# Kernel optimization log

Hardware: AMD Instinct MI355X
Metric: run time of the kernel (lower is better)

## Reference

```python
import jax, jax.numpy as jnp
import numpy as np

B, T, D = 4, 2048, 1024
H = 16
HD = D // H  # 64

def setup_inputs() -> dict:
    key = jax.random.key(0)
    k1, k2, k3 = jax.random.split(key, 3)
    x = jax.random.normal(k1, (B, T, D), dtype=jnp.float32)
    # torch nn.Linear weight layout: [out_features, in_features]
    w_qkv = jax.random.normal(k2, (3 * D, D), dtype=jnp.float32) * (D ** -0.5)
    w_proj = jax.random.normal(k3, (D, D), dtype=jnp.float32) * (D ** -0.5)
    return {"x": x, "w_qkv": w_qkv, "w_proj": w_proj}

def reference(x, w_qkv, w_proj):
    b, t, c = x.shape
    qkv = jnp.einsum('btc,oc->bto', x, w_qkv)  # [b,t,3c]
    q, k, v = jnp.split(qkv, 3, axis=-1)
    # [b,h,t,hd]
    q = q.reshape(b, t, H, HD).transpose(0, 2, 1, 3)
    k = k.reshape(b, t, H, HD).transpose(0, 2, 1, 3)
    v = v.reshape(b, t, H, HD).transpose(0, 2, 1, 3)
    att = jnp.einsum('bhqd,bhkd->bhqk', q, k) / (HD ** 0.5)
    causal = jnp.tril(jnp.ones((t, t), dtype=bool))
    att = jnp.where(causal, att, -jnp.inf)
    att = jax.nn.softmax(att, axis=-1)
    y = jnp.einsum('bhqk,bhkd->bhqd', att, v)
    y = y.transpose(0, 2, 1, 3).reshape(b, t, c)
    return jnp.einsum('btc,oc->bto', y, w_proj)
```

## Files before the change

kernel.cpp:

```cpp
#include <hip/hip_runtime.h>
#include <cstdint>
#include <cstddef>


typedef __bf16 bf16;
typedef __bf16 bf16x8 __attribute__((ext_vector_type(8)));
typedef float  f32x4  __attribute__((ext_vector_type(4)));
typedef float  fvec4  __attribute__((ext_vector_type(4)));
typedef unsigned u32x4 __attribute__((ext_vector_type(4)));

typedef __attribute__((address_space(1))) const void global_cv;
typedef __attribute__((address_space(3))) void lds_v;

#define MFMA16(a, b, c) __builtin_amdgcn_mfma_f32_16x16x32_bf16((a), (b), (c), 0, 0, 0)

#define QSCALE 0.18033688f

__device__ __forceinline__ void async_ld16(const bf16* g, bf16* l) {
  __builtin_amdgcn_global_load_lds((global_cv*)g, (lds_v*)l, 16, 0, 0);
}

__device__ __forceinline__ int swz_off(int row, int col) {
  int sr = (row & 7) ^ ((row >> 3) & 7);
  return row * 64 + ((((col >> 3) ^ sr) & 7) * 8) + (col & 7);
}

__device__ __forceinline__ bf16x8 cvt8(const float* p) {
  fvec4 u = *(const fvec4*)p;
  fvec4 v = *(const fvec4*)(p + 4);
  bf16x8 r;
  r[0] = (bf16)u[0]; r[1] = (bf16)u[1]; r[2] = (bf16)u[2]; r[3] = (bf16)u[3];
  r[4] = (bf16)v[0]; r[5] = (bf16)v[1]; r[6] = (bf16)v[2]; r[7] = (bf16)v[3];
  return r;
}

__global__ void cvt_f32_bf16(const float* __restrict__ s, bf16* __restrict__ d,
                             int n8) {
  int i = blockIdx.x * 256 + threadIdx.x;
  if (i < n8) *(bf16x8*)(d + (size_t)i * 8) = cvt8(s + (size_t)i * 8);
}

__device__ __forceinline__ void qkv_scatter(const f32x4 acc[4][4], int m0, int n0,
                                            int wm, int wn, int quad, int l15,
                                            bf16* Qo, bf16* Ko, bf16* Vo) {
  const int which = n0 >> 10;
  bf16* dst = (which == 0) ? Qo : (which == 1) ? Ko : Vo;
  const float scale = (which == 0) ? QSCALE : 1.0f;
#pragma unroll
  for (int i = 0; i < 4; ++i) {
    const int m = m0 + wm + i * 16 + quad * 4;
#pragma unroll
    for (int j = 0; j < 4; ++j) {
      const int n  = n0 + wn + j * 16 + l15;
      const int n1 = n & 1023;
      const int h  = n1 >> 6;
      const int d  = n1 & 63;
#pragma unroll
      for (int r = 0; r < 4; ++r) {
        const int mm = m + r;
        const int b  = mm >> 11;
        const int t  = mm & 2047;
        dst[(((size_t)(b * 16 + h)) * 2048 + t) * 64 + d] =
            (bf16)(acc[i][j][r] * scale);
      }
    }
  }
}

__global__ __launch_bounds__(256, 2)
void gemm_qkv_a(const bf16* __restrict__ A, const bf16* __restrict__ B,
                bf16* __restrict__ Qo, bf16* __restrict__ Ko,
                bf16* __restrict__ Vo) {
  __shared__ __align__(16) bf16 As[128 * 32];
  __shared__ __align__(16) bf16 Bs[128 * 32];
  const int K = 1024;

  const int tid  = threadIdx.x;
  const int lane = tid & 63;
  const int wave = tid >> 6;
  const int quad = lane >> 4;
  const int l15  = lane & 15;
  const int wm   = (wave >> 1) * 64;
  const int wn   = (wave & 1) * 64;
  const int m0   = blockIdx.y * 128;
  const int n0   = blockIdx.x * 128;

  f32x4 acc[4][4];
#pragma unroll
  for (int i = 0; i < 4; ++i)
#pragma unroll
    for (int j = 0; j < 4; ++j) acc[i][j] = f32x4{0.f, 0.f, 0.f, 0.f};

  const int r0 = tid >> 2;
  const int c0 = (tid & 3) * 8;
  const bf16* ag0 = A + (size_t)(m0 + r0) * K + c0;
  const bf16* ag1 = A + (size_t)(m0 + 64 + r0) * K + c0;
  const bf16* bg0 = B + (size_t)(n0 + r0) * K + c0;
  const bf16* bg1 = B + (size_t)(n0 + 64 + r0) * K + c0;
  const int lo0 = (wave * 64) * 8;
  const int lo1 = (256 + wave * 64) * 8;

  for (int k0 = 0; k0 < K; k0 += 32) {
    __syncthreads();
    async_ld16(ag0 + k0, As + lo0);
    async_ld16(ag1 + k0, As + lo1);
    async_ld16(bg0 + k0, Bs + lo0);
    async_ld16(bg1 + k0, Bs + lo1);
    __syncthreads();

    bf16x8 af[4], bfr[4];
#pragma unroll
    for (int i = 0; i < 4; ++i)
      af[i] = *(const bf16x8*)(As + (wm + i * 16 + l15) * 32 + quad * 8);
#pragma unroll
    for (int j = 0; j < 4; ++j)
      bfr[j] = *(const bf16x8*)(Bs + (wn + j * 16 + l15) * 32 + quad * 8);
#pragma unroll
    for (int i = 0; i < 4; ++i)
#pragma unroll
      for (int j = 0; j < 4; ++j)
        acc[i][j] = MFMA16(af[i], bfr[j], acc[i][j]);
  }
  qkv_scatter(acc, m0, n0, wm, wn, quad, l15, Qo, Ko, Vo);
}

__global__ __launch_bounds__(256, 2)
void gemm_qkv_f(const float* __restrict__ A, const float* __restrict__ B,
                bf16* __restrict__ Qo, bf16* __restrict__ Ko,
                bf16* __restrict__ Vo) {
  __shared__ __align__(16) bf16 As[128 * 32];
  __shared__ __align__(16) bf16 Bs[128 * 32];
  const int K = 1024;

  const int tid  = threadIdx.x;
  const int lane = tid & 63;
  const int wave = tid >> 6;
  const int quad = lane >> 4;
  const int l15  = lane & 15;
  const int wm   = (wave >> 1) * 64;
  const int wn   = (wave & 1) * 64;
  const int m0   = blockIdx.y * 128;
  const int n0   = blockIdx.x * 128;

  f32x4 acc[4][4];
#pragma unroll
  for (int i = 0; i < 4; ++i)
#pragma unroll
    for (int j = 0; j < 4; ++j) acc[i][j] = f32x4{0.f, 0.f, 0.f, 0.f};

  const int r0 = tid >> 2;
  const int c0 = (tid & 3) * 8;
  const size_t aoff0 = (size_t)(m0 + r0) * K + c0;
  const size_t aoff1 = (size_t)(m0 + 64 + r0) * K + c0;
  const size_t boff0 = (size_t)(n0 + r0) * K + c0;
  const size_t boff1 = (size_t)(n0 + 64 + r0) * K + c0;

  for (int k0 = 0; k0 < K; k0 += 32) {
    bf16x8 va0 = cvt8(A + aoff0 + k0);
    bf16x8 va1 = cvt8(A + aoff1 + k0);
    bf16x8 vb0 = cvt8(B + boff0 + k0);
    bf16x8 vb1 = cvt8(B + boff1 + k0);
    __syncthreads();
    *(bf16x8*)(As + tid * 8)        = va0;
    *(bf16x8*)(As + 2048 + tid * 8) = va1;
    *(bf16x8*)(Bs + tid * 8)        = vb0;
    *(bf16x8*)(Bs + 2048 + tid * 8) = vb1;
    __syncthreads();

    bf16x8 af[4], bfr[4];
#pragma unroll
    for (int i = 0; i < 4; ++i)
      af[i] = *(const bf16x8*)(As + (wm + i * 16 + l15) * 32 + quad * 8);
#pragma unroll
    for (int j = 0; j < 4; ++j)
      bfr[j] = *(const bf16x8*)(Bs + (wn + j * 16 + l15) * 32 + quad * 8);
#pragma unroll
    for (int i = 0; i < 4; ++i)
#pragma unroll
      for (int j = 0; j < 4; ++j)
        acc[i][j] = MFMA16(af[i], bfr[j], acc[i][j]);
  }
  qkv_scatter(acc, m0, n0, wm, wn, quad, l15, Qo, Ko, Vo);
}

__global__ __launch_bounds__(256, 2)
void attn(const bf16* __restrict__ Q, const bf16* __restrict__ Kk,
          const bf16* __restrict__ V, bf16* __restrict__ Y) {
  __shared__ __align__(16) bf16 Ks[2][64 * 64];
  __shared__ __align__(16) bf16 Vt[2][64 * 64];
  __shared__ __align__(16) bf16 Ps[4 * 16 * 64];

  const int tid  = threadIdx.x;
  const int wave = tid >> 6;
  const int lane = tid & 63;
  const int quad = lane >> 4;
  const int l15  = lane & 15;
  const int bh   = blockIdx.y;
  const int b    = bh >> 4;
  const int h    = bh & 15;
  const bf16* Qb = Q  + (size_t)bh * (2048 * 64);
  const bf16* Kb = Kk + (size_t)bh * (2048 * 64);
  const bf16* Vb = V  + (size_t)bh * (2048 * 64);
  bf16* Pw = Ps + wave * (16 * 64);

  const int kr = tid >> 2;
  const int kc = (tid & 3) * 16;
  const int vp = tid >> 3;
  const int vc8 = (tid & 7) * 8;

  const float NEG = -1e30f;

#pragma unroll 1
  for (int pass = 0; pass < 2; ++pass) {
    const int qt = pass ? (31 - (int)blockIdx.x) : (int)blockIdx.x;
    const int q0 = qt * 64;

    bf16x8 qa[2];
#pragma unroll
    for (int t = 0; t < 2; ++t)
      qa[t] = *(const bf16x8*)(Qb + (size_t)(q0 + wave * 16 + l15) * 64 + t * 32 + quad * 8);

    f32x4 l_run = {0.f, 0.f, 0.f, 0.f};
    f32x4 o[4];
#pragma unroll
    for (int j = 0; j < 4; ++j) o[j] = f32x4{0.f, 0.f, 0.f, 0.f};

    bf16x8 pk0 = *(const bf16x8*)(Kb + (size_t)kr * 64 + kc);
    bf16x8 pk1 = *(const bf16x8*)(Kb + (size_t)kr * 64 + kc + 8);
    u32x4  pva = *(const u32x4*)(Vb + (size_t)(2 * vp) * 64 + vc8);
    u32x4  pvb = *(const u32x4*)(Vb + (size_t)(2 * vp + 1) * 64 + vc8);

#pragma unroll 1
    for (int kt = 0; kt <= qt; ++kt) {
      const int cur = kt & 1;
      const int k0  = kt * 64;
      *(bf16x8*)(Ks[cur] + swz_off(kr, kc))     = pk0;
      *(bf16x8*)(Ks[cur] + swz_off(kr, kc + 8)) = pk1;
      {
        unsigned* vt32 = (unsigned*)Vt[cur];
#pragma unroll
        for (int i = 0; i < 8; ++i) {
          unsigned lo = (i & 1) ? (pva[i >> 1] >> 16) : (pva[i >> 1] & 0xFFFFu);
          unsigned hi = (i & 1) ? (pvb[i >> 1] >> 16) : (pvb[i >> 1] & 0xFFFFu);
          vt32[swz_off(vc8 + i, 2 * vp) >> 1] = lo | (hi << 16);
        }
      }
      __syncthreads();

      if (kt < qt) {
        const int kn = k0 + 64;
        pk0 = *(const bf16x8*)(Kb + (size_t)(kn + kr) * 64 + kc);
        pk1 = *(const bf16x8*)(Kb + (size_t)(kn + kr) * 64 + kc + 8);
        pva = *(const u32x4*)(Vb + (size_t)(kn + 2 * vp) * 64 + vc8);
        pvb = *(const u32x4*)(Vb + (size_t)(kn + 2 * vp + 1) * 64 + vc8);
      }

      f32x4 s[4];
#pragma unroll
      for (int j = 0; j < 4; ++j) {
        const int kvr = j * 16 + l15;
        bf16x8 k0f = *(const bf16x8*)(Ks[cur] + swz_off(kvr, quad * 8));
        bf16x8 k1f = *(const bf16x8*)(Ks[cur] + swz_off(kvr, 32 + quad * 8));
        f32x4 z = {0.f, 0.f, 0.f, 0.f};
        z = MFMA16(qa[0], k0f, z);
        z = MFMA16(qa[1], k1f, z);
        s[j] = z;
      }

      if (kt == qt) {
#pragma unroll
        for (int j = 0; j < 4; ++j) {
          const int kvg = k0 + j * 16 + l15;
#pragma unroll
          for (int r = 0; r < 4; ++r) {
            const int qg = q0 + wave * 16 + quad * 4 + r;
            if (kvg > qg) s[j][r] = NEG;
          }
        }
      }

#pragma unroll
      for (int j = 0; j < 4; ++j)
#pragma unroll
        for (int r = 0; r < 4; ++r) {
          float p = exp2f(s[j][r]);
          s[j][r] = p;
          l_run[r] += p;
        }

#pragma unroll
      for (int j = 0; j < 4; ++j)
#pragma unroll
        for (int r = 0; r < 4; ++r)
          Pw[swz_off(quad * 4 + r, j * 16 + l15)] = (bf16)s[j][r];

      bf16x8 pf0 = *(const bf16x8*)(Pw + swz_off(l15, quad * 8));
      bf16x8 pf1 = *(const bf16x8*)(Pw + swz_off(l15, 32 + quad * 8));
#pragma unroll
      for (int j = 0; j < 4; ++j) {
        const int d = j * 16 + l15;
        bf16x8 vf0 = *(const bf16x8*)(Vt[cur] + swz_off(d, quad * 8));
        bf16x8 vf1 = *(const bf16x8*)(Vt[cur] + swz_off(d, 32 + quad * 8));
        o[j] = MFMA16(pf0, vf0, o[j]);
        o[j] = MFMA16(pf1, vf1, o[j]);
      }
    }

#pragma unroll
    for (int msk = 1; msk < 16; msk <<= 1)
#pragma unroll
      for (int r = 0; r < 4; ++r) l_run[r] += __shfl_xor(l_run[r], msk);

#pragma unroll
    for (int j = 0; j < 4; ++j) {
      const int dcol = h * 64 + j * 16 + l15;
#pragma unroll
      for (int r = 0; r < 4; ++r) {
        const int trow = q0 + wave * 16 + quad * 4 + r;
        Y[((size_t)b * 2048 + trow) * 1024 + dcol] = (bf16)(o[j][r] / l_run[r]);
      }
    }
    __syncthreads();
  }
}

__global__ __launch_bounds__(256, 2)
void gemm_proj_a(const bf16* __restrict__ A, const bf16* __restrict__ B,
                 float* __restrict__ C) {
  __shared__ __align__(16) bf16 As[128 * 32];
  __shared__ __align__(16) bf16 Bs[128 * 32];
  const int K = 1024, N = 1024;

  const int tid  = threadIdx.x;
  const int lane = tid & 63;
  const int wave = tid >> 6;
  const int quad = lane >> 4;
  const int l15  = lane & 15;
  const int wm   = (wave >> 1) * 64;
  const int wn   = (wave & 1) * 64;
  const int m0   = blockIdx.y * 128;
  const int n0   = blockIdx.x * 128;

  f32x4 acc[4][4];
#pragma unroll
  for (int i = 0; i < 4; ++i)
#pragma unroll
    for (int j = 0; j < 4; ++j) acc[i][j] = f32x4{0.f, 0.f, 0.f, 0.f};

  const int r0 = tid >> 2;
  const int c0 = (tid & 3) * 8;
  const bf16* ag0 = A + (size_t)(m0 + r0) * K + c0;
  const bf16* ag1 = A + (size_t)(m0 + 64 + r0) * K + c0;
  const bf16* bg0 = B + (size_t)(n0 + r0) * K + c0;
  const bf16* bg1 = B + (size_t)(n0 + 64 + r0) * K + c0;
  const int lo0 = (wave * 64) * 8;
  const int lo1 = (256 + wave * 64) * 8;

  for (int k0 = 0; k0 < K; k0 += 32) {
    __syncthreads();
    async_ld16(ag0 + k0, As + lo0);
    async_ld16(ag1 + k0, As + lo1);
    async_ld16(bg0 + k0, Bs + lo0);
    async_ld16(bg1 + k0, Bs + lo1);
    __syncthreads();

    bf16x8 af[4], bfr[4];
#pragma unroll
    for (int i = 0; i < 4; ++i)
      af[i] = *(const bf16x8*)(As + (wm + i * 16 + l15) * 32 + quad * 8);
#pragma unroll
    for (int j = 0; j < 4; ++j)
      bfr[j] = *(const bf16x8*)(Bs + (wn + j * 16 + l15) * 32 + quad * 8);
#pragma unroll
    for (int i = 0; i < 4; ++i)
#pragma unroll
      for (int j = 0; j < 4; ++j)
        acc[i][j] = MFMA16(af[i], bfr[j], acc[i][j]);
  }

#pragma unroll
  for (int i = 0; i < 4; ++i) {
    const int m = m0 + wm + i * 16 + quad * 4;
#pragma unroll
    for (int j = 0; j < 4; ++j) {
      const int n = n0 + wn + j * 16 + l15;
#pragma unroll
      for (int r = 0; r < 4; ++r)
        C[(size_t)(m + r) * N + n] = acc[i][j][r];
    }
  }
}

__global__ __launch_bounds__(256, 2)
void gemm_proj_f(const bf16* __restrict__ A, const float* __restrict__ B,
                 float* __restrict__ C) {
  __shared__ __align__(16) bf16 As[128 * 32];
  __shared__ __align__(16) bf16 Bs[128 * 32];
  const int K = 1024, N = 1024;

  const int tid  = threadIdx.x;
  const int lane = tid & 63;
  const int wave = tid >> 6;
  const int quad = lane >> 4;
  const int l15  = lane & 15;
  const int wm   = (wave >> 1) * 64;
  const int wn   = (wave & 1) * 64;
  const int m0   = blockIdx.y * 128;
  const int n0   = blockIdx.x * 128;

  f32x4 acc[4][4];
#pragma unroll
  for (int i = 0; i < 4; ++i)
#pragma unroll
    for (int j = 0; j < 4; ++j) acc[i][j] = f32x4{0.f, 0.f, 0.f, 0.f};

  const int r0 = tid >> 2;
  const int c0 = (tid & 3) * 8;
  const size_t aoff0 = (size_t)(m0 + r0) * K + c0;
  const size_t aoff1 = (size_t)(m0 + 64 + r0) * K + c0;
  const size_t boff0 = (size_t)(n0 + r0) * K + c0;
  const size_t boff1 = (size_t)(n0 + 64 + r0) * K + c0;

  for (int k0 = 0; k0 < K; k0 += 32) {
    bf16x8 va0 = *(const bf16x8*)(A + aoff0 + k0);
    bf16x8 va1 = *(const bf16x8*)(A + aoff1 + k0);
    bf16x8 vb0 = cvt8(B + boff0 + k0);
    bf16x8 vb1 = cvt8(B + boff1 + k0);
    __syncthreads();
    *(bf16x8*)(As + tid * 8)        = va0;
    *(bf16x8*)(As + 2048 + tid * 8) = va1;
    *(bf16x8*)(Bs + tid * 8)        = vb0;
    *(bf16x8*)(Bs + 2048 + tid * 8) = vb1;
    __syncthreads();

    bf16x8 af[4], bfr[4];
#pragma unroll
    for (int i = 0; i < 4; ++i)
      af[i] = *(const bf16x8*)(As + (wm + i * 16 + l15) * 32 + quad * 8);
#pragma unroll
    for (int j = 0; j < 4; ++j)
      bfr[j] = *(const bf16x8*)(Bs + (wn + j * 16 + l15) * 32 + quad * 8);
#pragma unroll
    for (int i = 0; i < 4; ++i)
#pragma unroll
      for (int j = 0; j < 4; ++j)
        acc[i][j] = MFMA16(af[i], bfr[j], acc[i][j]);
  }

#pragma unroll
  for (int i = 0; i < 4; ++i) {
    const int m = m0 + wm + i * 16 + quad * 4;
#pragma unroll
    for (int j = 0; j < 4; ++j) {
      const int n = n0 + wn + j * 16 + l15;
#pragma unroll
      for (int r = 0; r < 4; ++r)
        C[(size_t)(m + r) * N + n] = acc[i][j][r];
    }
  }
}

extern "C" void kernel_launch(void* const* d_in, const int* in_sizes, int n_in,
                              void* d_out, int out_size, void* d_ws, size_t ws_size,
                              hipStream_t stream) {
  const float* x  = nullptr;
  const float* wq = nullptr;
  const float* wp = nullptr;
  for (int i = 0; i < n_in; ++i) {
    if      (in_sizes[i] == 8388608) x  = (const float*)d_in[i];
    else if (in_sizes[i] == 3145728) wq = (const float*)d_in[i];
    else if (in_sizes[i] == 1048576) wp = (const float*)d_in[i];
  }
  if (!x || !wq || !wp) {
    x = (const float*)d_in[0]; wq = (const float*)d_in[1]; wp = (const float*)d_in[2];
  }

  float* out = (float*)d_out;
  const size_t NE = (size_t)4 * 16 * 2048 * 64;
  bf16* kb = (bf16*)d_ws;
  bf16* vb = kb + NE;
  bf16* qb = vb + NE;
  bf16* yb = qb + NE;
  bf16* xb  = yb + NE;
  bf16* wqb = xb + 8388608;
  bf16* wpb = wqb + 3145728;
  const size_t need = (4 * NE + 8388608 + 3145728 + 1048576) * sizeof(bf16);
  const bool ext = ws_size >= need;

  if (ext) {
    cvt_f32_bf16<<<(8388608 / 8 + 255) / 256, 256, 0, stream>>>(x, xb, 8388608 / 8);
    cvt_f32_bf16<<<(3145728 / 8 + 255) / 256, 256, 0, stream>>>(wq, wqb, 3145728 / 8);
    cvt_f32_bf16<<<(1048576 / 8 + 255) / 256, 256, 0, stream>>>(wp, wpb, 1048576 / 8);
    gemm_qkv_a<<<dim3(24, 64), 256, 0, stream>>>(xb, wqb, qb, kb, vb);
  } else {
    gemm_qkv_f<<<dim3(24, 64), 256, 0, stream>>>(x, wq, qb, kb, vb);
  }

  attn<<<dim3(16, 64), 256, 0, stream>>>(qb, kb, vb, yb);

  if (ext) {
    gemm_proj_a<<<dim3(8, 64), 256, 0, stream>>>(yb, wpb, out);
  } else {
    gemm_proj_f<<<dim3(8, 64), 256, 0, stream>>>(yb, wp, out);
  }
}
```

Before: 278.1 us.

## Write V transposed from QKV GEMM and read K/V directly from global in attention

The QKV projection epilogue now writes V in a transposed [b,h,d,t] layout, so attention can load V fragments straight from global memory. The attention kernel drops its LDS staging of K and V, the in-kernel transpose and the per-tile barriers, and loads MFMA operands directly from global/L2. Block indices are remapped so that blocks sharing a head run close together for L2 reuse, and occupancy is raised to 4 blocks per CU. The risk is that each wave now fetches K/V redundantly from cache, adding global-load latency with no software prefetch to hide it.

```diff
diff --git a/kernel.cpp b/kernel.cpp
--- a/kernel.cpp
+++ b/kernel.cpp
@@ -4,6 +4,7 @@
 
 
 typedef __bf16 bf16;
+typedef __bf16 bf16x4 __attribute__((ext_vector_type(4)));
 typedef __bf16 bf16x8 __attribute__((ext_vector_type(8)));
 typedef float  f32x4  __attribute__((ext_vector_type(4)));
 typedef float  fvec4  __attribute__((ext_vector_type(4)));
@@ -44,7 +45,26 @@
                                             int wm, int wn, int quad, int l15,
                                             bf16* Qo, bf16* Ko, bf16* Vo) {
   const int which = n0 >> 10;
-  bf16* dst = (which == 0) ? Qo : (which == 1) ? Ko : Vo;
+  if (which == 2) {
+#pragma unroll
+    for (int i = 0; i < 4; ++i) {
+      const int m = m0 + wm + i * 16 + quad * 4;
+      const int b = m >> 11;
+      const int t = m & 2047;
+#pragma unroll
+      for (int j = 0; j < 4; ++j) {
+        const int n1 = (n0 + wn + j * 16 + l15) & 1023;
+        const int h  = n1 >> 6;
+        const int d  = n1 & 63;
+        bf16x4 v;
+#pragma unroll
+        for (int r = 0; r < 4; ++r) v[r] = (bf16)acc[i][j][r];
+        *(bf16x4*)(Vo + ((size_t)(b * 16 + h) * 64 + d) * 2048 + t) = v;
+      }
+    }
+    return;
+  }
+  bf16* dst = (which == 0) ? Qo : Ko;
   const float scale = (which == 0) ? QSCALE : 1.0f;
 #pragma unroll
   for (int i = 0; i < 4; ++i) {
@@ -183,11 +203,9 @@
   qkv_scatter(acc, m0, n0, wm, wn, quad, l15, Qo, Ko, Vo);
 }
 
-__global__ __launch_bounds__(256, 2)
+__global__ __launch_bounds__(256, 4)
 void attn(const bf16* __restrict__ Q, const bf16* __restrict__ Kk,
-          const bf16* __restrict__ V, bf16* __restrict__ Y) {
-  __shared__ __align__(16) bf16 Ks[2][64 * 64];
-  __shared__ __align__(16) bf16 Vt[2][64 * 64];
+          const bf16* __restrict__ Vt, bf16* __restrict__ Y) {
   __shared__ __align__(16) bf16 Ps[4 * 16 * 64];
 
   const int tid  = threadIdx.x;
@@ -195,75 +213,51 @@
   const int lane = tid & 63;
   const int quad = lane >> 4;
   const int l15  = lane & 15;
-  const int bh   = blockIdx.y;
+
+  const int lin  = (int)blockIdx.x + ((int)blockIdx.y << 4);
+  const int slot = lin >> 3;
+  const int bh   = (lin & 7) * 8 + (slot >> 4);
+  const int p    = slot & 15;
   const int b    = bh >> 4;
   const int h    = bh & 15;
+
   const bf16* Qb = Q  + (size_t)bh * (2048 * 64);
   const bf16* Kb = Kk + (size_t)bh * (2048 * 64);
-  const bf16* Vb = V  + (size_t)bh * (2048 * 64);
+  const bf16* Vb = Vt + (size_t)bh * (2048 * 64);
   bf16* Pw = Ps + wave * (16 * 64);
 
-  const int kr = tid >> 2;
-  const int kc = (tid & 3) * 16;
-  const int vp = tid >> 3;
-  const int vc8 = (tid & 7) * 8;
+  const bf16* kl = Kb + (size_t)l15 * 64 + quad * 8;
+  const bf16* vl = Vb + (size_t)l15 * 2048 + quad * 8;
 
   const float NEG = -1e30f;
 
 #pragma unroll 1
   for (int pass = 0; pass < 2; ++pass) {
-    const int qt = pass ? (31 - (int)blockIdx.x) : (int)blockIdx.x;
+    const int qt = pass ? (31 - p) : p;
     const int q0 = qt * 64;
 
-    bf16x8 qa[2];
-#pragma unroll
-    for (int t = 0; t < 2; ++t)
-      qa[t] = *(const bf16x8*)(Qb + (size_t)(q0 + wave * 16 + l15) * 64 + t * 32 + quad * 8);
+    const bf16* qp = Qb + (size_t)(q0 + wave * 16 + l15) * 64 + quad * 8;
+    bf16x8 qa0 = *(const bf16x8*)qp;
+    bf16x8 qa1 = *(const bf16x8*)(qp + 32);
 
     f32x4 l_run = {0.f, 0.f, 0.f, 0.f};
     f32x4 o[4];
 #pragma unroll
     for (int j = 0; j < 4; ++j) o[j] = f32x4{0.f, 0.f, 0.f, 0.f};
 
-    bf16x8 pk0 = *(const bf16x8*)(Kb + (size_t)kr * 64 + kc);
-    bf16x8 pk1 = *(const bf16x8*)(Kb + (size_t)kr * 64 + kc + 8);
-    u32x4  pva = *(const u32x4*)(Vb + (size_t)(2 * vp) * 64 + vc8);
-    u32x4  pvb = *(const u32x4*)(Vb + (size_t)(2 * vp + 1) * 64 + vc8);
-
 #pragma unroll 1
     for (int kt = 0; kt <= qt; ++kt) {
-      const int cur = kt & 1;
-      const int k0  = kt * 64;
-      *(bf16x8*)(Ks[cur] + swz_off(kr, kc))     = pk0;
-      *(bf16x8*)(Ks[cur] + swz_off(kr, kc + 8)) = pk1;
-      {
-        unsigned* vt32 = (unsigned*)Vt[cur];
-#pragma unroll
-        for (int i = 0; i < 8; ++i) {
-          unsigned lo = (i & 1) ? (pva[i >> 1] >> 16) : (pva[i >> 1] & 0xFFFFu);
-          unsigned hi = (i & 1) ? (pvb[i >> 1] >> 16) : (pvb[i >> 1] & 0xFFFFu);
-          vt32[swz_off(vc8 + i, 2 * vp) >> 1] = lo | (hi << 16);
-        }
-      }
-      __syncthreads();
-
-      if (kt < qt) {
-        const int kn = k0 + 64;
-        pk0 = *(const bf16x8*)(Kb + (size_t)(kn + kr) * 64 + kc);
-        pk1 = *(const bf16x8*)(Kb + (size_t)(kn + kr) * 64 + kc + 8);
-        pva = *(const u32x4*)(Vb + (size_t)(kn + 2 * vp) * 64 + vc8);
-        pvb = *(const u32x4*)(Vb + (size_t)(kn + 2 * vp + 1) * 64 + vc8);
-      }
+      const int k0 = kt * 64;
 
       f32x4 s[4];
 #pragma unroll
       for (int j = 0; j < 4; ++j) {
-        const int kvr = j * 16 + l15;
-        bf16x8 k0f = *(const bf16x8*)(Ks[cur] + swz_off(kvr, quad * 8));
-        bf16x8 k1f = *(const bf16x8*)(Ks[cur] + swz_off(kvr, 32 + quad * 8));
+        const bf16* kp = kl + (size_t)(k0 + j * 16) * 64;
+        bf16x8 k0f = *(const bf16x8*)kp;
+        bf16x8 k1f = *(const bf16x8*)(kp + 32);
         f32x4 z = {0.f, 0.f, 0.f, 0.f};
-        z = MFMA16(qa[0], k0f, z);
-        z = MFMA16(qa[1], k1f, z);
+        z = MFMA16(qa0, k0f, z);
+        z = MFMA16(qa1, k1f, z);
         s[j] = z;
       }
 
@@ -283,9 +277,9 @@
       for (int j = 0; j < 4; ++j)
 #pragma unroll
         for (int r = 0; r < 4; ++r) {
-          float p = exp2f(s[j][r]);
-          s[j][r] = p;
-          l_run[r] += p;
+          float pv = exp2f(s[j][r]);
+          s[j][r] = pv;
+          l_run[r] += pv;
         }
 
 #pragma unroll
@@ -296,11 +290,12 @@
 
       bf16x8 pf0 = *(const bf16x8*)(Pw + swz_off(l15, quad * 8));
       bf16x8 pf1 = *(const bf16x8*)(Pw + swz_off(l15, 32 + quad * 8));
+
 #pragma unroll
       for (int j = 0; j < 4; ++j) {
-        const int d = j * 16 + l15;
-        bf16x8 vf0 = *(const bf16x8*)(Vt[cur] + swz_off(d, quad * 8));
-        bf16x8 vf1 = *(const bf16x8*)(Vt[cur] + swz_off(d, 32 + quad * 8));
+        const bf16* vp = vl + (size_t)j * (16 * 2048) + k0;
+        bf16x8 vf0 = *(const bf16x8*)vp;
+        bf16x8 vf1 = *(const bf16x8*)(vp + 32);
         o[j] = MFMA16(pf0, vf0, o[j]);
         o[j] = MFMA16(pf1, vf1, o[j]);
       }
@@ -320,7 +315,6 @@
         Y[((size_t)b * 2048 + trow) * 1024 + dcol] = (bf16)(o[j][r] / l_run[r]);
       }
     }
-    __syncthreads();
   }
 }
 
```

Result: slower. 422.5 us (+51.9%).
